# Performance work log

Hardware: AMD Instinct MI355X
Metric: run time of the kernel (lower is better)

The kernel has to match this reference:

```python
import jax, jax.numpy as jnp
import numpy as np

B, D = 8192, 512
NB_CLASSES = 11318
N_EXP = 16
POS_THRESH = 0.25
TOP_K = int(round(B * POS_THRESH))  # plan==1: k = round(B * pos_thresh)


def make_bweights(n):
    # Deterministic init_bweights() from the torch module (17x17 for n=16).
    bw = np.zeros((n + 1, n + 1), dtype=np.float32)
    bw[:, 0] = -1.0 / n
    bw[0, 0] = 1.0
    for i in range(1, n + 1):
        for j in range(1, i):
            bw[i, j] = (-1.0 / n - bw[i] @ bw[j]) / bw[j, j]
        bw[i, i] = np.sqrt(1.0 - np.sum(bw[i, : i + 1] ** 2))
    bw[-1, -1] = 0.0
    return bw


def setup_inputs() -> dict:
    key = jax.random.key(0)
    k1, k2, k3, k4 = jax.random.split(key, 4)
    x_batch = jax.random.normal(k1, (B, D), jnp.float32)
    y_batch = jax.random.randint(k2, (B,), 0, NB_CLASSES)
    # kaiming_normal_ mode='fan_out' on a [nb_classes, sz_embed] tensor: std=sqrt(2/nb_classes)
    proxies = jax.random.normal(k3, (NB_CLASSES, D), jnp.float32) * np.float32(np.sqrt(2.0 / NB_CLASSES))
    rand_units = jax.random.normal(k4, (TOP_K, N_EXP, D), jnp.float32)
    rand_units = rand_units / jnp.linalg.norm(rand_units, axis=-1, keepdims=True)  # gen_unit()
    bweights = jnp.asarray(make_bweights(N_EXP))
    return {"x_batch": x_batch, "y_batch": y_batch, "proxies": proxies,
            "bweights": bweights, "rand_units": rand_units}


def _l2norm(x):
    # torch l2_norm: x / sqrt(sum(x^2, dim=1) + 1e-12)
    return x / jnp.sqrt(jnp.sum(x * x, axis=1, keepdims=True) + 1e-12)


def _expand_one(z, w_c, rands, bweights):
    # one2many_expansion for a single sample. z, w_c: [D]; rands: [N_EXP, D]
    M = jnp.dot(z, w_c) * w_c                 # projection onto class proxy
    r1 = z - M
    r1n = jnp.linalg.norm(r1)
    u1 = r1 / r1n
    # Build orthonormal basis v: [D, N_EXP+2]; columns 0,1 are w_c, u1,
    # columns 2.. via Gram-Schmidt on pre-drawn random unit vectors.
    v = jnp.zeros((D, N_EXP + 2), z.dtype).at[:, 0].set(w_c).at[:, 1].set(u1)
    for i in range(2, N_EXP + 2):  # fixed, small unrolled loop (16 steps)
        r = rands[i - 2]
        nb = r - v[:, :i] @ (v[:, :i].T @ r)  # == sum_j (r.b_j) b_j projection removal
        v = v.at[:, i].set(nb / jnp.linalg.norm(nb))
    # torch: v = v.clone().detach(); v[:,1] = u_1  (only u1 carries gradient)
    v = jax.lax.stop_gradient(v).at[:, 1].set(u1)
    u_rows = bweights @ v[:, 1:].T            # [N_EXP+1, D]
    z_exp = M[None, :] + u_rows * r1n         # [N_EXP+1, D]
    return z_exp[1:]                          # last N_EXP rows


def reference(x_batch, y_batch, proxies, bweights, rand_units):
    X = _l2norm(x_batch)                                  # keep_grad=True
    P = jax.lax.stop_gradient(_l2norm(proxies))           # .clone().detach()
    w = P[y_batch]                                        # [B, D] class proxies
    scores = jnp.sum(X * w, axis=1)                       # z @ P[lb]
    _, top_idx = jax.lax.top_k(scores, TOP_K)
    sel = jnp.sort(top_idx)  # torch loop appends expansions in ascending sample index order
    z_exp = jax.vmap(_expand_one, in_axes=(0, 0, 0, None))(X[sel], w[sel], rand_units, bweights)  # [TOP_K, N_EXP, D]
    lb_exp = jnp.repeat(y_batch[sel], N_EXP)
    aug_x = jnp.concatenate([x_batch, z_exp.reshape(-1, D)], axis=0)
    aug_t = jnp.concatenate([y_batch, lb_exp], axis=0)
    is_expan = jnp.zeros((B,), bool).at[sel].set(True)
    return aug_x, aug_t, is_expan
```

## Files before the change

kernel.cpp:

```cpp
#include <hip/hip_runtime.h>
#include <math.h>

#define BB     8192
#define DD     512
#define NEXP   16
#define TOPK   2048
#define AUGX_ROWS (BB + TOPK * NEXP)
#define AUGT_OFF  ((size_t)AUGX_ROWS * DD)
#define ISEXP_OFF (AUGT_OFF + AUGX_ROWS)

#define JCHUNK 256
#define COPY_BLOCKS 1024
#define BMP 520

typedef __attribute__((ext_vector_type(8)))  short bf16x8;
typedef __attribute__((ext_vector_type(16))) float f32x16;

__device__ inline ushort f2bf(float f) {
    uint u = __builtin_bit_cast(uint, f);
    return (ushort)((u + 0x7FFFu + ((u >> 16) & 1u)) >> 16);
}
__device__ inline float bf2f(ushort b) {
    uint u = ((uint)b) << 16;
    return __builtin_bit_cast(float, u);
}

__global__ __launch_bounds__(256) void score_kernel(
    const float* __restrict__ x, const int* __restrict__ y,
    const float* __restrict__ prox, double* __restrict__ scores,
    float4* __restrict__ hdr, int* __restrict__ ranks)
{
    int wave = threadIdx.x >> 6, lane = threadIdx.x & 63;
    int i = blockIdx.x * 4 + wave;
    const float* xr = x + (size_t)i * DD;
    const float* pr = prox + (size_t)y[i] * DD;
    double sx = 0.0, sp = 0.0, dp = 0.0;
    #pragma unroll
    for (int e = 0; e < DD; e += 64) {
        float xv = xr[e + lane];
        float pv = pr[e + lane];
        sx += (double)xv * (double)xv;
        sp += (double)pv * (double)pv;
        dp += (double)xv * (double)pv;
    }
    #pragma unroll
    for (int off = 32; off > 0; off >>= 1) {
        sx += __shfl_down(sx, off);
        sp += __shfl_down(sp, off);
        dp += __shfl_down(dp, off);
    }
    if (lane == 0) {
        double xn = sqrt(sx + 1e-12), pn = sqrt(sp + 1e-12);
        double zw = dp / (xn * pn);
        scores[i] = zw;
        double r1sq = 1.0 - zw * zw;
        if (r1sq < 1e-12) r1sq = 1e-12;
        float4 h = { (float)xn, (float)pn, (float)zw, (float)sqrt(r1sq) };
        hdr[i] = h;
        ranks[i] = 0;
    }
}

__global__ __launch_bounds__(256) void rank_kernel(
    const double* __restrict__ scores, int* __restrict__ ranks)
{
    __shared__ double ch[JCHUNK];
    int i = blockIdx.x * 256 + threadIdx.x;
    int jbase = blockIdx.y * JCHUNK;
    double si = scores[i];
    if (threadIdx.x < JCHUNK) ch[threadIdx.x] = scores[jbase + threadIdx.x];
    __syncthreads();
    int rank = 0;
    #pragma unroll 8
    for (int j = 0; j < JCHUNK; ++j) {
        double sj = ch[j];
        int jj = jbase + j;
        rank += (sj > si || (sj == si && jj < i)) ? 1 : 0;
    }
    atomicAdd(&ranks[i], rank);
}

__global__ __launch_bounds__(256) void compact_kernel(
    const int* __restrict__ ranks, int* __restrict__ sel, float* __restrict__ out)
{
    __shared__ int wsum[4];
    int t = threadIdx.x;
    int base = t * 32;
    int fl[32];
    int cnt = 0;
    #pragma unroll
    for (int q = 0; q < 8; ++q) {
        int4 rv = *(const int4*)&ranks[base + q * 4];
        fl[q * 4 + 0] = (rv.x < TOPK) ? 1 : 0;
        fl[q * 4 + 1] = (rv.y < TOPK) ? 1 : 0;
        fl[q * 4 + 2] = (rv.z < TOPK) ? 1 : 0;
        fl[q * 4 + 3] = (rv.w < TOPK) ? 1 : 0;
        cnt += fl[q*4] + fl[q*4+1] + fl[q*4+2] + fl[q*4+3];
    }
    int lane = t & 63, wave = t >> 6;
    int inc = cnt;
    #pragma unroll
    for (int off = 1; off < 64; off <<= 1) {
        int n = __shfl_up(inc, off);
        if (lane >= off) inc += n;
    }
    if (lane == 63) wsum[wave] = inc;
    __syncthreads();
    int wbase = 0;
    for (int w = 0; w < wave; ++w) wbase += wsum[w];
    int pos = wbase + inc - cnt;
    #pragma unroll
    for (int q = 0; q < 8; ++q) {
        float4 ev = { fl[q*4] ? 1.0f : 0.0f, fl[q*4+1] ? 1.0f : 0.0f,
                      fl[q*4+2] ? 1.0f : 0.0f, fl[q*4+3] ? 1.0f : 0.0f };
        *(float4*)&out[ISEXP_OFF + base + q * 4] = ev;
        #pragma unroll
        for (int i = 0; i < 4; ++i)
            if (fl[q * 4 + i]) sel[pos++] = base + q * 4 + i;
    }
}

__global__ __launch_bounds__(256, 7) void expand_kernel(
    const float* __restrict__ x, const int* __restrict__ y,
    const float* __restrict__ prox, const float* __restrict__ bwg,
    const float* __restrict__ rands, const int* __restrict__ sel,
    const float4* __restrict__ hdr, float* __restrict__ out)
{
    const int t = threadIdx.x;
    const int q = blockIdx.x / 3, r3 = blockIdx.x % 3;

    if (r3 == 2) {
        int tid = q * 256 + t;
        const float4* src = (const float4*)x;
        float4* dst = (float4*)out;
        const int nvec = BB * DD / 4;
        for (int idx = tid; idx < nvec; idx += COPY_BLOCKS * 256) dst[idx] = src[idx];
        for (int i = tid; i < BB; i += COPY_BLOCKS * 256) out[AUGT_OFF + i] = (float)y[i];
        return;
    }

    __shared__ ushort Bm[18][BMP];
    union SPool {
        float Gp[2][18][19];
        struct { float Ls[18][19]; float Cs[16][18]; } s;
    };
    __shared__ SPool pool;

    const int j = 2 * q + r3;
    const int wave = t >> 6, lane = t & 63;
    const int s = sel[j];
    const int cls = y[s];

    {
        const float* rbase = rands + (size_t)j * NEXP * DD;
        #pragma unroll
        for (int i = 0; i < 8; ++i) {
            int row = 2 * i + (t >> 7);
            int col = (t & 127) * 4;
            float4 vv = *(const float4*)(rbase + (size_t)row * DD + col);
            ushort4 bv = { f2bf(vv.x), f2bf(vv.y), f2bf(vv.z), f2bf(vv.w) };
            *(ushort4*)&Bm[2 + row][col] = bv;
        }
    }

    float4 h = hdr[s];
    const float zw = h.z, r1n = h.w;
    const float ixn = 1.0f / h.x, ipn = 1.0f / h.y, ir1 = 1.0f / r1n;

    float2 xv = ((const float2*)(x + (size_t)s * DD))[t];
    float2 pv = ((const float2*)(prox + (size_t)cls * DD))[t];
    float2 w  = { pv.x * ipn, pv.y * ipn };
    float2 z  = { xv.x * ixn, xv.y * ixn };
    float2 M  = { zw * w.x, zw * w.y };
    float2 u1 = { (z.x - M.x) * ir1, (z.y - M.y) * ir1 };

    { ushort2 wb = { f2bf(w.x),  f2bf(w.y)  }; *(ushort2*)&Bm[0][2 * t] = wb; }
    { ushort2 ub = { f2bf(u1.x), f2bf(u1.y) }; *(ushort2*)&Bm[1][2 * t] = ub; }

    if (t < NEXP) out[AUGT_OFF + BB + (size_t)j * NEXP + t] = (float)cls;
    __syncthreads();

    if (wave < 2) {
        int row = lane & 31; if (row > 17) row = 17;
        int koff = (lane >> 5) * 8;
        const int kw = wave * 256;
        f32x16 acc = {0,0,0,0,0,0,0,0,0,0,0,0,0,0,0,0};
        #pragma unroll
        for (int stp = 0; stp < 16; ++stp) {
            bf16x8 av = *(const bf16x8*)&Bm[row][kw + stp * 16 + koff];
            acc = __builtin_amdgcn_mfma_f32_32x32x16_bf16(av, av, acc, 0, 0, 0);
        }
        int col = lane & 31;
        if (col < 18) {
            #pragma unroll
            for (int rg = 0; rg < 16; ++rg) {
                int rr = (rg & 3) + 8 * (rg >> 2) + 4 * (lane >> 5);
                if (rr < 18) pool.Gp[wave][rr][col] = acc[rg];
            }
        }
    }
    __syncthreads();

    if (wave == 0) {
        const int jl = (lane < 18) ? lane : 17;
        float Greg[18];
        #pragma unroll
        for (int c = 0; c < 18; ++c)
            Greg[c] = pool.Gp[0][jl][c] + pool.Gp[1][jl][c];

        float Lrow[18], idr[18];
        #pragma unroll
        for (int col = 0; col < 18; ++col) {
            float pivot = __shfl(Greg[col], col);
            float rsq = rsqrtf(pivot);
            idr[col] = rsq;
            float lv = (jl >= col) ? Greg[col] * rsq : 0.0f;
            Lrow[col] = lv;
            #pragma unroll
            for (int c = col + 1; c < 18; ++c) {
                float lc = __shfl(lv, c);
                Greg[c] -= lv * lc;
            }
        }
        #pragma unroll
        for (int c = 0; c < 18; ++c) pool.s.Ls[jl][c] = Lrow[c];

        if (lane < 16) {
            float b[18];
            b[0] = 0.0f;
            #pragma unroll
            for (int m = 1; m < 18; ++m) b[m] = bwg[17 + lane * 17 + (m - 1)];
            #pragma unroll
            for (int k = 17; k >= 0; --k) {
                float xk = b[k] * idr[k];
                pool.s.Cs[lane][k] = xk;
                #pragma unroll
                for (int m = 0; m < k; ++m)
                    b[m] -= pool.s.Ls[k][m] * xk;
            }
        }
    }
    __syncthreads();

    float bx[18], by[18];
    #pragma unroll
    for (int jj = 0; jj < 18; ++jj) {
        uint v = *(const uint*)&Bm[jj][2 * t];
        bx[jj] = bf2f((ushort)(v & 0xffffu));
        by[jj] = bf2f((ushort)(v >> 16));
    }

    float* orow = out + ((size_t)BB + (size_t)j * NEXP) * DD;
    #pragma unroll
    for (int half = 0; half < 2; ++half) {
        float acc0[8], acc1[8];
        #pragma unroll
        for (int r = 0; r < 8; ++r) { acc0[r] = 0.0f; acc1[r] = 0.0f; }
        #pragma unroll
        for (int jj = 0; jj < 18; ++jj) {
            #pragma unroll
            for (int r = 0; r < 8; ++r) {
                float cc = pool.s.Cs[half * 8 + r][jj];
                acc0[r] += cc * bx[jj];
                acc1[r] += cc * by[jj];
            }
        }
        #pragma unroll
        for (int r = 0; r < 8; ++r) {
            float2 ov = { M.x + r1n * acc0[r], M.y + r1n * acc1[r] };
            ((float2*)(orow + (size_t)(half * 8 + r) * DD))[t] = ov;
        }
    }
}

extern "C" void kernel_launch(void* const* d_in, const int* in_sizes, int n_in,
                              void* d_out, int out_size, void* d_ws, size_t ws_size,
                              hipStream_t stream)
{
    const float* x     = (const float*)d_in[0];
    const int*   y     = (const int*)d_in[1];
    const float* prox  = (const float*)d_in[2];
    const float* bw    = (const float*)d_in[3];
    const float* rands = (const float*)d_in[4];
    float* out = (float*)d_out;

    char* wsb = (char*)d_ws;
    double* scores = (double*)wsb;
    int* ranks = (int*)(wsb + 65536);
    int* sel   = (int*)(wsb + 65536 + 32768);
    float4* hdr = (float4*)(wsb + 114688);

    score_kernel<<<BB / 4, 256, 0, stream>>>(x, y, prox, scores, hdr, ranks);
    dim3 rgrid(BB / 256, BB / JCHUNK);
    rank_kernel<<<rgrid, 256, 0, stream>>>(scores, ranks);
    compact_kernel<<<1, 256, 0, stream>>>(ranks, sel, out);
    expand_kernel<<<TOPK + COPY_BLOCKS, 256, 0, stream>>>(x, y, prox, bw, rands,
                                                          sel, hdr, out);
}
```

Baseline: 61.72 us.

## Compute Cholesky solve redundantly in every wave and broadcast via shuffles

Each of the four waves now runs the 18x18 Cholesky factorisation and the triangular solve itself. L and the solved coefficients stay in registers and are exchanged through lane shuffles, replacing the shared-memory Ls/Cs tables and one __syncthreads. This removes a barrier where three waves idled while wave 0 worked, and it frees shared memory. The cost is redundant ALU work in every wave and many more cross-lane shuffles, including 288 shuffles per half in the output accumulation loop where there were shared-memory broadcast reads before.

Measured after the change: 143.6 us. +132.7%, slower.

```diff
diff --git a/kernel.cpp b/kernel.cpp
--- a/kernel.cpp
+++ b/kernel.cpp
@@ -140,11 +140,7 @@
     }
 
     __shared__ ushort Bm[18][BMP];
-    union SPool {
-        float Gp[2][18][19];
-        struct { float Ls[18][19]; float Cs[16][18]; } s;
-    };
-    __shared__ SPool pool;
+    __shared__ float Gp[2][18][19];
 
     const int j = 2 * q + r3;
     const int wave = t >> 6, lane = t & 63;
@@ -195,52 +191,49 @@
             #pragma unroll
             for (int rg = 0; rg < 16; ++rg) {
                 int rr = (rg & 3) + 8 * (rg >> 2) + 4 * (lane >> 5);
-                if (rr < 18) pool.Gp[wave][rr][col] = acc[rg];
+                if (rr < 18) Gp[wave][rr][col] = acc[rg];
             }
         }
     }
     __syncthreads();
 
-    if (wave == 0) {
-        const int jl = (lane < 18) ? lane : 17;
-        float Greg[18];
-        #pragma unroll
-        for (int c = 0; c < 18; ++c)
-            Greg[c] = pool.Gp[0][jl][c] + pool.Gp[1][jl][c];
-
-        float Lrow[18], idr[18];
-        #pragma unroll
-        for (int col = 0; col < 18; ++col) {
-            float pivot = __shfl(Greg[col], col);
-            float rsq = rsqrtf(pivot);
-            idr[col] = rsq;
-            float lv = (jl >= col) ? Greg[col] * rsq : 0.0f;
-            Lrow[col] = lv;
+    const int jl = (lane < 18) ? lane : 17;
+    float Greg[18];
+    #pragma unroll
+    for (int c = 0; c < 18; ++c)
+        Greg[c] = Gp[0][jl][c] + Gp[1][jl][c];
+
+    float Lrow[18], idr[18];
+    #pragma unroll
+    for (int col = 0; col < 18; ++col) {
+        float pivot = __shfl(Greg[col], col);
+        float rsq = rsqrtf(pivot);
+        idr[col] = rsq;
+        float lv = (jl >= col) ? Greg[col] * rsq : 0.0f;
+        Lrow[col] = lv;
+        #pragma unroll
+        for (int c = col + 1; c < 18; ++c) {
+            float lc = __shfl(lv, c);
+            Greg[c] -= lv * lc;
+        }
+    }
+
+    float xreg[18];
+    {
+        float b[18];
+        b[0] = 0.0f;
+        int rsel = (lane < 16) ? lane : 0;
+        #pragma unroll
+        for (int m = 1; m < 18; ++m) b[m] = bwg[17 + rsel * 17 + (m - 1)];
+        #pragma unroll
+        for (int k = 17; k >= 0; --k) {
+            float xk = b[k] * idr[k];
+            xreg[k] = xk;
             #pragma unroll
-            for (int c = col + 1; c < 18; ++c) {
-                float lc = __shfl(lv, c);
-                Greg[c] -= lv * lc;
-            }
-        }
-        #pragma unroll
-        for (int c = 0; c < 18; ++c) pool.s.Ls[jl][c] = Lrow[c];
-
-        if (lane < 16) {
-            float b[18];
-            b[0] = 0.0f;
-            #pragma unroll
-            for (int m = 1; m < 18; ++m) b[m] = bwg[17 + lane * 17 + (m - 1)];
-            #pragma unroll
-            for (int k = 17; k >= 0; --k) {
-                float xk = b[k] * idr[k];
-                pool.s.Cs[lane][k] = xk;
-                #pragma unroll
-                for (int m = 0; m < k; ++m)
-                    b[m] -= pool.s.Ls[k][m] * xk;
-            }
-        }
-    }
-    __syncthreads();
+            for (int m = 0; m < k; ++m)
+                b[m] -= __shfl(Lrow[m], k) * xk;
+        }
+    }
 
     float bx[18], by[18];
     #pragma unroll
@@ -258,11 +251,12 @@
         for (int r = 0; r < 8; ++r) { acc0[r] = 0.0f; acc1[r] = 0.0f; }
         #pragma unroll
         for (int jj = 0; jj < 18; ++jj) {
+            float cx = bx[jj], cy = by[jj];
             #pragma unroll
             for (int r = 0; r < 8; ++r) {
-                float cc = pool.s.Cs[half * 8 + r][jj];
-                acc0[r] += cc * bx[jj];
-                acc1[r] += cc * by[jj];
+                float cc = __shfl(xreg[jj], half * 8 + r);
+                acc0[r] += cc * cx;
+                acc1[r] += cc * cy;
             }
         }
         #pragma unroll
```
